# Performance work log

Measured on AMD Instinct MI355X. Metric: run time of the kernel, lower is better.

The kernel has to match this reference:

```python
import jax, jax.numpy as jnp
import numpy as np

B, S, D = 2, 2048, 1024
H = 8
HD = D // H  # 128
RANK = 4
CONTROL_SCALE = 1.0


def setup_inputs() -> dict:
    key = jax.random.key(0)
    ks = jax.random.split(key, 8)
    sd = 0.02
    return {
        "hidden_states": jax.random.normal(ks[0], (B, S, D), jnp.float32),
        "control_states": jax.random.normal(ks[1], (B, S, D), jnp.float32),
        "Wq": jax.random.normal(ks[2], (D, D), jnp.float32) * sd,
        "Wk": jax.random.normal(ks[3], (D, D), jnp.float32) * sd,
        "Wv": jax.random.normal(ks[4], (D, D), jnp.float32) * sd,
        "Wo": jax.random.normal(ks[5], (D, D), jnp.float32) * sd,
        "bo": jnp.zeros((D,), jnp.float32),
        "lora_down": jax.random.normal(ks[6], (RANK, D), jnp.float32) * sd,
        "lora_up": jax.random.normal(ks[7], (D, RANK), jnp.float32) * sd,
    }


def _split_heads(x):  # [B,S,D] -> [B,H,S,HD]
    return x.reshape(B, S, H, HD).transpose(0, 2, 1, 3)


def reference(hidden_states, control_states, Wq, Wk, Wv, Wo, bo, lora_down, lora_up):
    # q/k/v projections (Linear, no bias); self-attention (encoder_hidden_states=None)
    q = _split_heads(jnp.einsum("bsd,ed->bse", hidden_states, Wq))
    k = _split_heads(jnp.einsum("bsd,ed->bse", hidden_states, Wk))
    v = _split_heads(jnp.einsum("bsd,ed->bse", hidden_states, Wv))
    inv_sqrt_d = 1.0 / jnp.sqrt(jnp.asarray(HD, q.dtype))
    scores = jnp.einsum("bhqd,bhkd->bhqk", q, k) * inv_sqrt_d  # [B,H,S,S]
    probs = jax.nn.softmax(scores, axis=-1)
    attn_out = jnp.einsum("bhqk,bhkd->bhqd", probs, v)  # [B,H,S,HD]
    attn_out = attn_out.transpose(0, 2, 1, 3).reshape(B, S, D)
    # to_out[0] Linear with bias; to_out[1] Dropout is identity at eval
    out = jnp.einsum("bsd,ed->bse", attn_out, Wo) + bo
    # LoRA control injection: up(down(control_states))
    ctrl = jnp.einsum("bsr,er->bse", jnp.einsum("bsd,rd->bsr", control_states, lora_down), lora_up)
    return out + CONTROL_SCALE * ctrl
```

## Files before the change

### kernel.cpp

```cpp
#include <hip/hip_runtime.h>
#include <hip/hip_bf16.h>


typedef __bf16 bf8_t __attribute__((ext_vector_type(8)));
typedef float f32x4 __attribute__((ext_vector_type(4)));
typedef float f32x16 __attribute__((ext_vector_type(16)));
typedef unsigned u32x4 __attribute__((ext_vector_type(4)));

#define MFMA16(a, b, c) __builtin_amdgcn_mfma_f32_16x16x32_bf16((a), (b), (c), 0, 0, 0)
#define MFMA32(a, b, c) __builtin_amdgcn_mfma_f32_32x32x16_bf16((a), (b), (c), 0, 0, 0)

__device__ __forceinline__ void gload_lds16(const void* g, void* l) {
  __builtin_amdgcn_global_load_lds(
      (const __attribute__((address_space(1))) void*)g,
      (__attribute__((address_space(3))) void*)l, 16, 0, 0);
}

__device__ __forceinline__ unsigned pk2(float a, float b) {
  unsigned short ua = __builtin_bit_cast(unsigned short, (__bf16)a);
  unsigned short ub = __builtin_bit_cast(unsigned short, (__bf16)b);
  return (unsigned)ua | ((unsigned)ub << 16);
}

__device__ __forceinline__ float fmax3(float a, float b, float c) {
  return fmaxf(fmaxf(a, b), c);
}

__global__ __launch_bounds__(256) void cvt5_k(
    const float* __restrict__ s0, const float* __restrict__ s1,
    const float* __restrict__ s2, const float* __restrict__ s3,
    const float* __restrict__ s4, __bf16* __restrict__ d0,
    __bf16* __restrict__ d1, __bf16* __restrict__ d2, __bf16* __restrict__ d3,
    __bf16* __restrict__ d4) {
  const int which = blockIdx.y;
  const float* s = (which == 0) ? s0 : (which == 1) ? s1 : (which == 2) ? s2
                   : (which == 3) ? s3 : s4;
  __bf16* d = (which == 0) ? d0 : (which == 1) ? d1 : (which == 2) ? d2
              : (which == 3) ? d3 : d4;
  const int n = (which == 0) ? (4096 * 1024) : (1024 * 1024);
  const int i = (blockIdx.x * 256 + threadIdx.x) * 8;
  if (i >= n) return;
  float4 a = *(const float4*)(s + i);
  float4 b = *(const float4*)(s + i + 4);
  bf8_t r;
  r[0] = (__bf16)a.x; r[1] = (__bf16)a.y; r[2] = (__bf16)a.z; r[3] = (__bf16)a.w;
  r[4] = (__bf16)b.x; r[5] = (__bf16)b.y; r[6] = (__bf16)b.z; r[7] = (__bf16)b.w;
  *(bf8_t*)(d + i) = r;
}

template <int MR>
__device__ __forceinline__ void gemm_tile(const __bf16* __restrict__ Abase,
                                          const __bf16* __restrict__ Wbase,
                                          int K, __bf16* sA, __bf16* sB,
                                          f32x4 acc[MR][4]) {
  const int tid = threadIdx.x;
  const int wave = tid >> 6, lane = tid & 63;
  const int wr = (wave >> 1) * (MR * 16), wc = (wave & 1) * 64;
  const int lrow = lane >> 3, lchunk = lane & 7;

  for (int m = 0; m < MR; ++m)
    for (int n = 0; n < 4; ++n)
      acc[m][n] = f32x4{0.f, 0.f, 0.f, 0.f};

  for (int k0 = 0; k0 < K; k0 += 64) {
    for (int i = 0; i < MR; ++i) {
      const int rbase = i * 32 + wave * 8;
      gload_lds16(Abase + (size_t)(rbase + lrow) * K + k0 + lchunk * 8,
                  sA + rbase * 64);
    }
    for (int i = 0; i < 4; ++i) {
      const int rbase = i * 32 + wave * 8;
      gload_lds16(Wbase + (size_t)(rbase + lrow) * K + k0 + lchunk * 8,
                  sB + rbase * 64);
    }
    __syncthreads();

    for (int kk = 0; kk < 2; ++kk) {
      bf8_t af[MR], bfr[4];
      const int koff = kk * 32 + (lane >> 4) * 8;
      for (int m = 0; m < MR; ++m)
        af[m] = *(const bf8_t*)&sA[(wr + m * 16 + (lane & 15)) * 64 + koff];
      for (int n = 0; n < 4; ++n)
        bfr[n] = *(const bf8_t*)&sB[(wc + n * 16 + (lane & 15)) * 64 + koff];
      for (int m = 0; m < MR; ++m)
        for (int n = 0; n < 4; ++n)
          acc[m][n] = MFMA16(af[m], bfr[n], acc[m][n]);
    }
    __syncthreads();
  }
}

__global__ __launch_bounds__(256) void gemm_qkv_k(
    const __bf16* __restrict__ X, const __bf16* __restrict__ Wq,
    const __bf16* __restrict__ Wk, const __bf16* __restrict__ Wv,
    __bf16* __restrict__ Qb, __bf16* __restrict__ Kb, __bf16* __restrict__ Vtb) {
  __shared__ __bf16 sA[128 * 64];
  __shared__ __bf16 sB[128 * 64];
  const int lin = blockIdx.x + 8 * (blockIdx.y + 32 * blockIdx.z);
  const int p8 = lin & 7;
  const int rest = lin >> 3;
  const int p32 = rest & 31;
  const int z = rest >> 5;
  const int K = 1024;
  int rowT, colT, Nout;
  const __bf16 *Abase, *Wbase;
  __bf16* C;
  if (z == 2) {
    rowT = p8; colT = p32; Nout = 4096;
    Abase = Wv + (size_t)rowT * 128 * K;
    Wbase = X + (size_t)colT * 128 * K;
    C = Vtb;
  } else {
    rowT = p32; colT = p8; Nout = 1024;
    Abase = X + (size_t)rowT * 128 * K;
    Wbase = ((z == 0) ? Wq : Wk) + (size_t)colT * 128 * K;
    C = (z == 0) ? Qb : Kb;
  }
  f32x4 acc[4][4];
  gemm_tile<4>(Abase, Wbase, K, sA, sB, acc);

  const int lane = threadIdx.x & 63, wave = threadIdx.x >> 6;
  const int wr = (wave >> 1) * 64, wc = (wave & 1) * 64;
  const int row0 = rowT * 128 + wr + (lane >> 4) * 4;
  const int col0 = colT * 128 + wc + (lane & 15);
  for (int m = 0; m < 4; ++m)
    for (int n = 0; n < 4; ++n)
      for (int j = 0; j < 4; ++j)
        C[(size_t)(row0 + m * 16 + j) * Nout + col0 + n * 16] = (__bf16)acc[m][n][j];
}

__global__ __launch_bounds__(256) void lora_down_k(
    const float* __restrict__ ctrl, const float* __restrict__ down,
    float* __restrict__ tmp) {
  const int tid = threadIdx.x, wave = tid >> 6, lane = tid & 63;
  const int s = blockIdx.x * 4 + wave;
  const float* cp = ctrl + (size_t)s * 1024 + lane * 16;
  float4 c[4];
  for (int i = 0; i < 4; ++i) c[i] = *(const float4*)(cp + i * 4);
  for (int r = 0; r < 4; ++r) {
    const float* dp = down + r * 1024 + lane * 16;
    float acc = 0.f;
    for (int i = 0; i < 4; ++i) {
      float4 dv = *(const float4*)(dp + i * 4);
      acc += c[i].x * dv.x + c[i].y * dv.y + c[i].z * dv.z + c[i].w * dv.w;
    }
    for (int off = 32; off > 0; off >>= 1) acc += __shfl_xor(acc, off);
    if (lane == 0) tmp[s * 4 + r] = acc;
  }
}

__global__ __launch_bounds__(256) void flash_attn_k(
    const __bf16* __restrict__ Qg, const __bf16* __restrict__ Kg,
    const __bf16* __restrict__ Vtg, __bf16* __restrict__ Op,
    float* __restrict__ ml) {
  const int S = 2048, D = 1024;
  const int NT = 16;
  __shared__ __bf16 sK[2][32 * 128];
  __shared__ __bf16 sVt[2][128 * 32];
  __shared__ float sW[4][32];

  const int lin = blockIdx.x + 16 * (blockIdx.y + 16 * blockIdx.z);
  const int bh = (lin & 7) * 2 + ((lin >> 9) & 1);
  const int qt = (lin >> 3) & 15;
  const int z = (lin >> 7) & 3;

  const int b = bh >> 3, h = bh & 7;
  const int tid = threadIdx.x, wave = tid >> 6, lane = tid & 63;
  const int l31 = lane & 31, hi = lane >> 5;
  const size_t base = (size_t)b * S * D + (size_t)h * 128;
  const size_t vtbase = (size_t)h * 128 * 4096 + (size_t)b * 2048;
  const int q0 = qt * 128 + wave * 32;
  const int kvofs = z * 512;

  bf8_t qf[8];
  {
    const float c = 0.08838834764831845f * 1.4426950408889634f;
    const __bf16* qp = Qg + base + (size_t)(q0 + l31) * D + hi * 8;
#pragma unroll
    for (int dc = 0; dc < 8; ++dc) {
      bf8_t v = *(const bf8_t*)(qp + dc * 16);
#pragma unroll
      for (int j = 0; j < 8; ++j) v[j] = (__bf16)((float)v[j] * c);
      qf[dc] = v;
    }
  }

  f32x16 accO[4];
#pragma unroll
  for (int db = 0; db < 4; ++db)
#pragma unroll
    for (int j = 0; j < 16; ++j) accO[db][j] = 0.f;
  float m_ = -1e30f, l_ = 0.f;

  auto stageK = [&](int buf, int kv) {
#pragma unroll
    for (int i = 0; i < 2; ++i) {
      const int r = wave * 8 + i * 4 + (lane >> 4);
      const int gc = (lane & 15) ^ (r & 7);
      gload_lds16(Kg + base + (size_t)(kvofs + kv + r) * D + gc * 8,
                  &sK[buf][(wave * 8 + i * 4) * 128]);
    }
  };
  auto stageV = [&](int buf, int kv) {
#pragma unroll
    for (int i = 0; i < 2; ++i) {
      const int d = wave * 32 + i * 16 + (lane >> 2);
      const int gc = (lane & 3) ^ ((d >> 1) & 3);
      gload_lds16(Vtg + vtbase + (size_t)d * 4096 + kvofs + kv + gc * 8,
                  &sVt[buf][(wave * 32 + i * 16) * 32]);
    }
  };

  stageK(0, 0);
  stageV(0, 0);

  for (int t = 0; t < NT; ++t) {
    const int cur = t & 1;
    __syncthreads();
    if (t < NT - 1) {
      stageK(cur ^ 1, (t + 1) * 32);
      stageV(cur ^ 1, (t + 1) * 32);
    }

    f32x16 accS;
#pragma unroll
    for (int j = 0; j < 16; ++j) accS[j] = 0.f;
    const __bf16* kb_ = sK[cur];
    const int kr = l31;
    __builtin_amdgcn_s_setprio(1);
#pragma unroll
    for (int dc = 0; dc < 8; ++dc) {
      bf8_t a = *(const bf8_t*)&kb_[kr * 128 + ((2 * dc + hi) ^ (kr & 7)) * 8];
      accS = MFMA32(a, qf[dc], accS);
    }
    __builtin_amdgcn_s_setprio(0);

    float pm;
    {
      float t0 = fmax3(accS[0], accS[1], accS[2]);
      float t1 = fmax3(accS[3], accS[4], accS[5]);
      float t2 = fmax3(accS[6], accS[7], accS[8]);
      float t3 = fmax3(accS[9], accS[10], accS[11]);
      float t4 = fmax3(accS[12], accS[13], accS[14]);
      pm = fmax3(fmax3(t0, t1, t2), fmax3(t3, t4, accS[15]),
                 __builtin_inff() * -1.0f);
      pm = fmaxf(pm, __shfl_xor(pm, 32));
    }

    if (__ballot(pm > m_ + 8.0f)) {
      const float mn = fmaxf(m_, pm);
      const float sc = exp2f(m_ - mn);
      m_ = mn;
      l_ *= sc;
      if (hi == 0) sW[wave][l31] = sc;
#pragma unroll
      for (int r = 0; r < 16; ++r) {
        const float scr = sW[wave][(r & 3) + 8 * (r >> 2) + 4 * hi];
#pragma unroll
        for (int db = 0; db < 4; ++db) accO[db][r] *= scr;
      }
    }

    float sm[16];
#pragma unroll
    for (int j = 0; j < 16; ++j) {
      const float p = exp2f(accS[j] - m_);
      accS[j] = p;
      sm[j] = p;
    }
#pragma unroll
    for (int j = 0; j < 8; ++j) sm[j] += sm[j + 8];
#pragma unroll
    for (int j = 0; j < 4; ++j) sm[j] += sm[j + 4];
    l_ += (sm[0] + sm[1]) + (sm[2] + sm[3]);

    unsigned pk[4][2];
#pragma unroll
    for (int tq = 0; tq < 4; ++tq) {
      pk[tq][0] = pk2(accS[4 * tq + 0], accS[4 * tq + 1]);
      pk[tq][1] = pk2(accS[4 * tq + 2], accS[4 * tq + 3]);
    }

    const __bf16* vt_ = sVt[cur];
#pragma unroll
    for (int kc = 0; kc < 2; ++kc) {
      const unsigned own0 = hi ? pk[2 * kc + 1][0] : pk[2 * kc][0];
      const unsigned own1 = hi ? pk[2 * kc + 1][1] : pk[2 * kc][1];
      const unsigned snd0 = hi ? pk[2 * kc][0] : pk[2 * kc + 1][0];
      const unsigned snd1 = hi ? pk[2 * kc][1] : pk[2 * kc + 1][1];
      const unsigned rc0 = (unsigned)__shfl_xor((int)snd0, 32);
      const unsigned rc1 = (unsigned)__shfl_xor((int)snd1, 32);
      u32x4 fr;
      fr[0] = hi ? rc0 : own0;
      fr[1] = hi ? rc1 : own1;
      fr[2] = hi ? own0 : rc0;
      fr[3] = hi ? own1 : rc1;
      const bf8_t pa = __builtin_bit_cast(bf8_t, fr);
      __builtin_amdgcn_s_setprio(1);
#pragma unroll
      for (int db = 0; db < 4; ++db) {
        const int dr = db * 32 + l31;
        const int p = (kc * 2 + hi) ^ ((dr >> 1) & 3);
        bf8_t vb = *(const bf8_t*)&vt_[dr * 32 + p * 8];
        accO[db] = MFMA32(pa, vb, accO[db]);
      }
      __builtin_amdgcn_s_setprio(0);
    }
  }

  const float lf = l_ + __shfl_xor(l_, 32);

  const size_t pbase = ((size_t)(z * 16 + bh) * 2048 + q0);
#pragma unroll
  for (int r = 0; r < 16; ++r) {
    const int qr = (r & 3) + 8 * (r >> 2) + 4 * hi;
    __bf16* op = Op + (pbase + qr) * 128 + l31;
#pragma unroll
    for (int db = 0; db < 4; ++db)
      op[db * 32] = (__bf16)(accO[db][r]);
  }
  if (hi == 0) {
    ml[(pbase + l31) * 2 + 0] = m_;
    ml[(pbase + l31) * 2 + 1] = lf;
  }
}

__global__ __launch_bounds__(256) void attn_merge_k(
    const __bf16* __restrict__ Op, const float* __restrict__ ml,
    __bf16* __restrict__ Og) {
  const int bh = blockIdx.x >> 7, qc = blockIdx.x & 127;
  const int t = threadIdx.x;
  const int qr = qc * 16 + (t >> 4);
  const int d0 = (t & 15) * 8;
  const int b = bh >> 3, h = bh & 7;

  size_t idx[4];
  float mi[4], li[4];
  float m = -1e30f;
#pragma unroll
  for (int i = 0; i < 4; ++i) {
    idx[i] = ((size_t)(i * 16 + bh) * 2048 + qr);
    mi[i] = ml[idx[i] * 2];
    li[i] = ml[idx[i] * 2 + 1];
    m = fmaxf(m, mi[i]);
  }
  float den = 0.f, w[4];
#pragma unroll
  for (int i = 0; i < 4; ++i) {
    w[i] = exp2f(mi[i] - m);
    den += li[i] * w[i];
  }
  const float inv = 1.0f / den;

  float acc[8] = {0, 0, 0, 0, 0, 0, 0, 0};
#pragma unroll
  for (int i = 0; i < 4; ++i) {
    bf8_t o = *(const bf8_t*)(Op + idx[i] * 128 + d0);
#pragma unroll
    for (int j = 0; j < 8; ++j) acc[j] += (float)o[j] * w[i];
  }
  bf8_t r;
#pragma unroll
  for (int j = 0; j < 8; ++j) r[j] = (__bf16)(acc[j] * inv);
  *(bf8_t*)(Og + ((size_t)(b * 2048 + qr) * 1024) + h * 128 + d0) = r;
}

__global__ __launch_bounds__(256) void gemm_out_k(
    const __bf16* __restrict__ A, const __bf16* __restrict__ Wo,
    const float* __restrict__ bo, const float* __restrict__ lup,
    const float* __restrict__ tmp, float* __restrict__ out) {
  __shared__ __bf16 sA[64 * 64];
  __shared__ __bf16 sB[128 * 64];
  const int lin = blockIdx.x + 8 * blockIdx.y;
  const int bcol = lin & 7;
  const int brow = lin >> 3;
  const int K = 1024, N = 1024;
  f32x4 acc[2][4];
  gemm_tile<2>(A + (size_t)brow * 64 * K, Wo + (size_t)bcol * 128 * K, K, sA, sB, acc);

  const int lane = threadIdx.x & 63, wave = threadIdx.x >> 6;
  const int wr = (wave >> 1) * 32, wc = (wave & 1) * 64;
  for (int n = 0; n < 4; ++n) {
    const int col = bcol * 128 + wc + n * 16 + (lane & 15);
    const float bias = bo[col];
    const float u0 = lup[col * 4 + 0], u1 = lup[col * 4 + 1];
    const float u2 = lup[col * 4 + 2], u3 = lup[col * 4 + 3];
    for (int m = 0; m < 2; ++m)
      for (int j = 0; j < 4; ++j) {
        const int row = brow * 64 + wr + m * 16 + (lane >> 4) * 4 + j;
        const float* t = tmp + row * 4;
        float v = acc[m][n][j] + bias + t[0] * u0 + t[1] * u1 + t[2] * u2 + t[3] * u3;
        out[(size_t)row * N + col] = v;
      }
  }
}

extern "C" void kernel_launch(void* const* d_in, const int* in_sizes, int n_in,
                              void* d_out, int out_size, void* d_ws, size_t ws_size,
                              hipStream_t stream) {
  (void)in_sizes; (void)n_in; (void)out_size; (void)ws_size;
  const float* hs  = (const float*)d_in[0];
  const float* cs  = (const float*)d_in[1];
  const float* Wq  = (const float*)d_in[2];
  const float* Wk  = (const float*)d_in[3];
  const float* Wv  = (const float*)d_in[4];
  const float* Wo  = (const float*)d_in[5];
  const float* bo  = (const float*)d_in[6];
  const float* ldw = (const float*)d_in[7];
  const float* lup = (const float*)d_in[8];
  float* out = (float*)d_out;

  const size_t MD = (size_t)4096 * 1024;
  const size_t WD = (size_t)1024 * 1024;
  __bf16* hsb = (__bf16*)d_ws;
  __bf16* Wqb = hsb + MD;
  __bf16* Wkb = Wqb + WD;
  __bf16* Wvb = Wkb + WD;
  __bf16* Wob = Wvb + WD;
  __bf16* Qb  = Wob + WD;
  __bf16* Kb  = Qb + MD;
  __bf16* Vtb = Kb + MD;
  __bf16* Ab  = Vtb + MD;
  float*  tmp = (float*)(Ab + MD);
  __bf16* Opart = (__bf16*)(tmp + 4096 * 4);
  float*  mlp   = (float*)(Opart + (size_t)4 * 16 * 2048 * 128);

  cvt5_k<<<dim3(2048, 5), 256, 0, stream>>>(hs, Wq, Wk, Wv, Wo,
                                            hsb, Wqb, Wkb, Wvb, Wob);
  gemm_qkv_k<<<dim3(8, 32, 3), 256, 0, stream>>>(hsb, Wqb, Wkb, Wvb, Qb, Kb, Vtb);
  lora_down_k<<<dim3(1024), 256, 0, stream>>>(cs, ldw, tmp);
  flash_attn_k<<<dim3(16, 16, 4), 256, 0, stream>>>(Qb, Kb, Vtb, Opart, mlp);
  attn_merge_k<<<dim3(2048), 256, 0, stream>>>(Opart, mlp, Ab);
  gemm_out_k<<<dim3(8, 64), 256, 0, stream>>>(Ab, Wob, bo, lup, tmp, out);
}
```

Before: 161.5 us.

## Compact convert grid, drop setprio in attention, vectorize out-GEMM epilogue loads

The conversion kernel now uses a flat grid of exactly the needed blocks instead of a 2048x5 grid, where most blocks for the weight matrices exited early. The s_setprio hints around the MFMA loops in flash attention are removed. The output GEMM epilogue loads LoRA tmp rows and lora_up values as float4 once, instead of as scalar loads inside the loop. These are three small, independent tweaks aimed at launch waste, scheduling and load count.

```diff
diff --git a/kernel.cpp b/kernel.cpp
--- a/kernel.cpp
+++ b/kernel.cpp
@@ -32,14 +32,20 @@
     const float* __restrict__ s4, __bf16* __restrict__ d0,
     __bf16* __restrict__ d1, __bf16* __restrict__ d2, __bf16* __restrict__ d3,
     __bf16* __restrict__ d4) {
-  const int which = blockIdx.y;
+  const int blk = blockIdx.x;
+  int which, off;
+  if (blk < 2048) {
+    which = 0; off = blk;
+  } else {
+    const int w = blk - 2048;
+    which = 1 + (w >> 9);
+    off = w & 511;
+  }
   const float* s = (which == 0) ? s0 : (which == 1) ? s1 : (which == 2) ? s2
                    : (which == 3) ? s3 : s4;
   __bf16* d = (which == 0) ? d0 : (which == 1) ? d1 : (which == 2) ? d2
               : (which == 3) ? d3 : d4;
-  const int n = (which == 0) ? (4096 * 1024) : (1024 * 1024);
-  const int i = (blockIdx.x * 256 + threadIdx.x) * 8;
-  if (i >= n) return;
+  const int i = (off * 256 + threadIdx.x) * 8;
   float4 a = *(const float4*)(s + i);
   float4 b = *(const float4*)(s + i + 4);
   bf8_t r;
@@ -227,13 +233,11 @@
     for (int j = 0; j < 16; ++j) accS[j] = 0.f;
     const __bf16* kb_ = sK[cur];
     const int kr = l31;
-    __builtin_amdgcn_s_setprio(1);
 #pragma unroll
     for (int dc = 0; dc < 8; ++dc) {
       bf8_t a = *(const bf8_t*)&kb_[kr * 128 + ((2 * dc + hi) ^ (kr & 7)) * 8];
       accS = MFMA32(a, qf[dc], accS);
     }
-    __builtin_amdgcn_s_setprio(0);
 
     float pm;
     {
@@ -296,7 +300,6 @@
       fr[2] = hi ? own0 : rc0;
       fr[3] = hi ? own1 : rc1;
       const bf8_t pa = __builtin_bit_cast(bf8_t, fr);
-      __builtin_amdgcn_s_setprio(1);
 #pragma unroll
       for (int db = 0; db < 4; ++db) {
         const int dr = db * 32 + l31;
@@ -304,7 +307,6 @@
         bf8_t vb = *(const bf8_t*)&vt_[dr * 32 + p * 8];
         accO[db] = MFMA32(pa, vb, accO[db]);
       }
-      __builtin_amdgcn_s_setprio(0);
     }
   }
 
@@ -380,17 +382,28 @@
 
   const int lane = threadIdx.x & 63, wave = threadIdx.x >> 6;
   const int wr = (wave >> 1) * 32, wc = (wave & 1) * 64;
+
+  float4 tv[2][4];
+  int rows[2][4];
+#pragma unroll
+  for (int m = 0; m < 2; ++m)
+#pragma unroll
+    for (int j = 0; j < 4; ++j) {
+      rows[m][j] = brow * 64 + wr + m * 16 + (lane >> 4) * 4 + j;
+      tv[m][j] = *(const float4*)(tmp + rows[m][j] * 4);
+    }
+
   for (int n = 0; n < 4; ++n) {
     const int col = bcol * 128 + wc + n * 16 + (lane & 15);
     const float bias = bo[col];
-    const float u0 = lup[col * 4 + 0], u1 = lup[col * 4 + 1];
-    const float u2 = lup[col * 4 + 2], u3 = lup[col * 4 + 3];
+    const float4 u = *(const float4*)(lup + col * 4);
+#pragma unroll
     for (int m = 0; m < 2; ++m)
+#pragma unroll
       for (int j = 0; j < 4; ++j) {
-        const int row = brow * 64 + wr + m * 16 + (lane >> 4) * 4 + j;
-        const float* t = tmp + row * 4;
-        float v = acc[m][n][j] + bias + t[0] * u0 + t[1] * u1 + t[2] * u2 + t[3] * u3;
-        out[(size_t)row * N + col] = v;
+        const float4 t = tv[m][j];
+        float v = acc[m][n][j] + bias + t.x * u.x + t.y * u.y + t.z * u.z + t.w * u.w;
+        out[(size_t)rows[m][j] * N + col] = v;
       }
   }
 }
@@ -425,8 +438,8 @@
   __bf16* Opart = (__bf16*)(tmp + 4096 * 4);
   float*  mlp   = (float*)(Opart + (size_t)4 * 16 * 2048 * 128);
 
-  cvt5_k<<<dim3(2048, 5), 256, 0, stream>>>(hs, Wq, Wk, Wv, Wo,
-                                            hsb, Wqb, Wkb, Wvb, Wob);
+  cvt5_k<<<dim3(4096), 256, 0, stream>>>(hs, Wq, Wk, Wv, Wo,
+                                         hsb, Wqb, Wkb, Wvb, Wob);
   gemm_qkv_k<<<dim3(8, 32, 3), 256, 0, stream>>>(hsb, Wqb, Wkb, Wvb, Qb, Kb, Vtb);
   lora_down_k<<<dim3(1024), 256, 0, stream>>>(cs, ldw, tmp);
   flash_attn_k<<<dim3(16, 16, 4), 256, 0, stream>>>(Qb, Kb, Vtb, Opart, mlp);
```

Result: no change. 158.5 us (-1.9%).
